# Kernel tuning notes

Measured on AMD Instinct MI355X. Metric: run time of the kernel, lower is better.

## Reference

```python
import jax, jax.numpy as jnp
import numpy as np
from jax import lax

BN_EPS = 1e-5


def _conv_bn_relu(x, W, b, gamma, beta):
    # x: [B, Cin, N]; W: [Cout, Cin]; 1x1 conv == channel GEMM
    y = jnp.einsum('oc,bcn->bon', W, x) + b[None, :, None]
    mean = jnp.mean(y, axis=(0, 2), keepdims=True)
    var = jnp.mean((y - mean) ** 2, axis=(0, 2), keepdims=True)  # biased, torch BN train mode
    y = gamma[None, :, None] * (y - mean) / jnp.sqrt(var + BN_EPS) + beta[None, :, None]
    return jax.nn.relu(y)


def setup_inputs() -> dict:
    key = jax.random.key(0)
    ks = jax.random.split(key, 8)
    B, N1, N2, C1, C2 = 16, 4096, 1024, 128, 256
    Cin, H = C1 + C2, 256  # MLP dims [384, 256, 256]
    inp = {
        'centroids1': jax.random.normal(ks[0], (B, 3, N1), jnp.float32),
        'centroids2': jax.random.normal(ks[1], (B, 3, N2), jnp.float32),
        'features1': jax.random.normal(ks[2], (B, C1, N1), jnp.float32),
        'features2': jax.random.normal(ks[3], (B, C2, N2), jnp.float32),
        'W1': jax.random.normal(ks[4], (H, Cin), jnp.float32) / np.sqrt(Cin),
        'b1': jnp.zeros((H,), jnp.float32),
        'g1': jnp.ones((H,), jnp.float32),
        'be1': jnp.zeros((H,), jnp.float32),
        'W2': jax.random.normal(ks[5], (H, H), jnp.float32) / np.sqrt(H),
        'b2': jnp.zeros((H,), jnp.float32),
        'g2': jnp.ones((H,), jnp.float32),
        'be2': jnp.zeros((H,), jnp.float32),
    }
    return inp


def reference(centroids1, centroids2, features1, features2,
              W1, b1, g1, be1, W2, b2, g2, be2):
    c1 = centroids1.transpose(0, 2, 1)  # [B, N1, 3]
    c2 = centroids2.transpose(0, 2, 1)  # [B, N2, 3]
    f2 = features2.transpose(0, 2, 1)   # [B, N2, C2]

    # pairwise squared distances [B, N1, N2]
    d = (jnp.sum(c1 ** 2, -1)[:, :, None] + jnp.sum(c2 ** 2, -1)[:, None, :]
         - 2.0 * jnp.einsum('bnd,bmd->bnm', c1, c2))

    # 3 nearest neighbors (smallest distances)
    neg_top, idx = lax.top_k(-d, 3)            # idx: [B, N1, 3]
    dist3 = -neg_top
    recip = 1.0 / (dist3 + 1e-8)
    weight = recip / jnp.sum(recip, axis=2, keepdims=True)  # [B, N1, 3]

    gathered = jax.vmap(lambda f, i: f[i])(f2, idx)         # [B, N1, 3, C2]
    interp = jnp.sum(gathered * weight[..., None], axis=2)  # [B, N1, C2]

    feats = jnp.concatenate((features1.transpose(0, 2, 1), interp), axis=-1)  # [B, N1, C1+C2]
    x = feats.transpose(0, 2, 1)  # [B, C1+C2, N1]
    x = _conv_bn_relu(x, W1, b1, g1, be1)
    x = _conv_bn_relu(x, W2, b2, g2, be2)
    return x  # [B, 256, N1]
```

## Files before the change

kernel.cpp:

```cpp
#include <hip/hip_runtime.h>
#include <math.h>

#define N1 4096
#define N2 1024
#define C1 128
#define C2 256
#define CIN 384
#define H 256
#define BATCH 16
#define BN_EPS 1e-5f

typedef __attribute__((ext_vector_type(8))) short bf16x8;
typedef __attribute__((ext_vector_type(4))) float f32x4;

__device__ inline float bf2f(short s) {
    union { unsigned u; float f; } x;
    x.u = ((unsigned)(unsigned short)s) << 16;
    return x.f;
}
__device__ inline short f2bf(float f) {
    union { float f; unsigned u; } x; x.f = f;
    unsigned r = x.u + 0x7fffu + ((x.u >> 16) & 1u);
    return (short)(r >> 16);
}

typedef const __attribute__((address_space(1))) unsigned int guint;
typedef __attribute__((address_space(3))) unsigned int luint;
__device__ inline void gll16(const void* g, void* l) {
    __builtin_amdgcn_global_load_lds((guint*)g, (luint*)l, 16, 0, 0);
}

__global__ __launch_bounds__(256)
void knn_kernel(const float* __restrict__ c1, const float* __restrict__ c2,
                float4* __restrict__ pk) {
    __shared__ __align__(16) float4 sc[N2];
    __shared__ float md[64 * 13];
    __shared__ int   mi[64 * 13];
    const int b = blockIdx.y;
    const float* c2b = c2 + (size_t)b * 3 * N2;
    for (int j = threadIdx.x; j < N2; j += 256) {
        float xx = c2b[j], yy = c2b[N2 + j], zz = c2b[2 * N2 + j];
        sc[j] = make_float4(xx, yy, zz, xx * xx + yy * yy + zz * zz);
    }
    __syncthreads();

    const int t = threadIdx.x;
    const int q = t & 63;
    const int quarter = t >> 6;
    const int n = blockIdx.x * 64 + q;
    const float* c1b = c1 + (size_t)b * 3 * N1;
    const float x = c1b[n], y = c1b[N1 + n], z = c1b[2 * N1 + n];
    const float s1 = x * x + y * y + z * z;

    float d0 = 3.4e38f, d1 = 3.4e38f, d2 = 3.4e38f;
    int i0 = 0, i1 = 0, i2 = 0;
    const int j0 = quarter * 256;
    #pragma unroll 4
    for (int jj = 0; jj < 256; ++jj) {
        const int j = j0 + jj;
        float4 cc = sc[j];
        float dot = x * cc.x + y * cc.y + z * cc.z;
        float d = s1 + cc.w - 2.0f * dot;
        bool c0 = d < d0, c1v = d < d1, c2v = d < d2;
        d2 = c1v ? d1 : (c2v ? d : d2);  i2 = c1v ? i1 : (c2v ? j : i2);
        d1 = c0 ? d0 : (c1v ? d : d1);   i1 = c0 ? i0 : (c1v ? j : i1);
        d0 = c0 ? d  : d0;               i0 = c0 ? j  : i0;
    }
    const int mb = q * 13 + quarter * 3;
    md[mb + 0] = d0; md[mb + 1] = d1; md[mb + 2] = d2;
    mi[mb + 0] = i0; mi[mb + 1] = i1; mi[mb + 2] = i2;
    __syncthreads();

    if (t < 64) {
        float e0 = 3.4e38f, e1 = 3.4e38f, e2 = 3.4e38f;
        int a0 = 0, a1 = 0, a2 = 0;
        #pragma unroll
        for (int r = 0; r < 12; ++r) {
            const int rr = t * 13 + (r / 3) * 3 + (r % 3);
            float d = md[rr]; int j = mi[rr];
            bool c0 = d < e0, c1v = d < e1, c2v = d < e2;
            e2 = c1v ? e1 : (c2v ? d : e2);  a2 = c1v ? a1 : (c2v ? j : a2);
            e1 = c0 ? e0 : (c1v ? d : e1);   a1 = c0 ? a0 : (c1v ? j : a1);
            e0 = c0 ? d  : e0;               a0 = c0 ? j  : a0;
        }
        float r0 = 1.0f / (e0 + 1e-8f);
        float r1 = 1.0f / (e1 + 1e-8f);
        float r2 = 1.0f / (e2 + 1e-8f);
        float rs = r0 + r1 + r2;
        unsigned pack = (unsigned)a0 | ((unsigned)a1 << 10) | ((unsigned)a2 << 20);
        pk[(size_t)b * N1 + n] = make_float4(__uint_as_float(pack), r0 / rs, r1 / rs, r2 / rs);
    }
}

__global__ __launch_bounds__(256)
void prep_w(const float* __restrict__ W, short* __restrict__ Wsw, int K) {
    const int nkb = K >> 3;
    const int id = blockIdx.x * 256 + threadIdx.x;
    if (id >= 256 * nkb) return;
    const int m = id / nkb, kb = id % nkb;
    const float* src = W + (size_t)m * K + kb * 8;
    bf16x8 v;
    #pragma unroll
    for (int j = 0; j < 8; ++j) v[j] = f2bf(src[j]);
    *(bf16x8*)(Wsw + ((size_t)kb * 256 + m) * 8) = v;
}

__global__ __launch_bounds__(256)
void transpose_f2(const float* __restrict__ f2, short* __restrict__ f2t) {
    __shared__ float st[32][33];
    const int j0 = blockIdx.x * 32, c0 = blockIdx.y * 32, b = blockIdx.z;
    const int t = threadIdx.x;
    {
        const int cc = t >> 3, jj = (t & 7) * 4;
        const float* src = f2 + ((size_t)b * C2 + c0 + cc) * N2 + j0 + jj;
        float4 v = *(const float4*)src;
        st[cc][jj + 0] = v.x; st[cc][jj + 1] = v.y;
        st[cc][jj + 2] = v.z; st[cc][jj + 3] = v.w;
    }
    __syncthreads();
    {
        const int j = t >> 3, cb = (t & 7) * 4;
        short4 v = { f2bf(st[cb + 0][j]), f2bf(st[cb + 1][j]),
                     f2bf(st[cb + 2][j]), f2bf(st[cb + 3][j]) };
        *(short4*)(f2t + ((size_t)b * N2 + j0 + j) * C2 + c0 + cb) = v;
    }
}

template<int MODE>
__global__ __launch_bounds__(512)
void gemm_kernel(const short* __restrict__ Wsw,
                 const float* __restrict__ X0, const short* __restrict__ X1,
                 const float4* __restrict__ pk,
                 const float* __restrict__ scale, const float* __restrict__ shift,
                 short* __restrict__ Ykc, float2* __restrict__ P) {
    constexpr int K = (MODE == 0) ? CIN : H;
    constexpr int NT = K / 32;

    __shared__ __align__(16) short A_lds[2][4][256][8];
    __shared__ __align__(16) short B_lds[2][4][128][8];
    __shared__ float sc_s[256], sh_s[256];
    __shared__ float2 pb[256][2];

    const int t = threadIdx.x;
    const int n0 = blockIdx.x * 128;
    const int b  = blockIdx.y;
    const int blkid = b * 32 + blockIdx.x;

    if (MODE == 1 && t < 256) { sc_s[t] = scale[t]; sh_s[t] = shift[t]; }

    const int sn  = t & 127;
    const int skb = t >> 7;
    const int lane = t & 63, wv = t >> 6;
    const int wm = wv >> 1, wn = wv & 1;
    const int l16 = lane & 15, lq = lane >> 4;
    const int am_base = wm * 64 + l16;
    const int bn_base = wn * 64 + l16;

    const float* X0b = (MODE == 0) ? X0 + (size_t)b * C1 * N1 : (const float*)nullptr;
    const short* f2tb = (MODE == 0) ? X1 + (size_t)b * N2 * C2 : (const short*)nullptr;
    const short* y1b  = (MODE == 1) ? X1 + (size_t)b * 32 * N1 * 8 : (const short*)nullptr;

    int gi0 = 0, gi1 = 0, gi2 = 0;
    float gw0 = 0.f, gw1 = 0.f, gw2 = 0.f;
    if (MODE == 0) {
        float4 v = pk[(size_t)b * N1 + n0 + sn];
        unsigned u = __float_as_uint(v.x);
        gi0 = u & 1023; gi1 = (u >> 10) & 1023; gi2 = (u >> 20) & 1023;
        gw0 = v.y; gw1 = v.z; gw2 = v.w;
    }

    f32x4 acc[4][4];
    #pragma unroll
    for (int i = 0; i < 4; ++i)
        #pragma unroll
        for (int j = 0; j < 4; ++j)
            acc[i][j] = (f32x4){0.f, 0.f, 0.f, 0.f};

    auto stageA = [&](int step, int bufi) {
        const short* g = Wsw + (size_t)step * 8192 + wv * 512 + lane * 8;
        short* l = &A_lds[bufi][0][0][0] + wv * 512;
        gll16(g, l);
        gll16(g + 4096, l + 4096);
    };

    auto compute = [&](int bufi) {
        bf16x8 a[4], bb[4];
        #pragma unroll
        for (int f = 0; f < 4; ++f) {
            a[f]  = *(const bf16x8*)&A_lds[bufi][lq][am_base + f * 16][0];
            bb[f] = *(const bf16x8*)&B_lds[bufi][lq][bn_base + f * 16][0];
        }
        #pragma unroll
        for (int i = 0; i < 4; ++i)
            #pragma unroll
            for (int j = 0; j < 4; ++j)
                acc[i][j] = __builtin_amdgcn_mfma_f32_16x16x32_bf16(a[i], bb[j], acc[i][j], 0, 0, 0);
    };

    __syncthreads();

    {
        float pf[8]; bf16x8 pg0, pg1, pg2, py;
        if (MODE == 0) {
            const float* src = X0b + (size_t)(skb * 8) * N1 + n0 + sn;
            #pragma unroll
            for (int j = 0; j < 8; ++j) pf[j] = src[(size_t)j * N1];
        } else {
            py = *(const bf16x8*)(y1b + ((size_t)skb * N1 + n0 + sn) * 8);
        }
        stageA(0, 0);
        bf16x8 pv;
        if (MODE == 0) {
            #pragma unroll
            for (int j = 0; j < 8; ++j) pv[j] = f2bf(pf[j]);
        } else {
            const int gk = skb * 8;
            #pragma unroll
            for (int e = 0; e < 8; ++e)
                pv[e] = f2bf(fmaxf(fmaf(bf2f(py[e]), sc_s[gk + e], sh_s[gk + e]), 0.f));
        }
        *(bf16x8*)&B_lds[0][skb][sn][0] = pv;
        (void)pg0; (void)pg1; (void)pg2;
    }
    __syncthreads();

    int buf = 0;
    for (int s = 0; s < NT; ++s) {
        const bool has_next = (s + 1 < NT);
        const bool nearly = (MODE == 0) && (s + 1 < 4);
        float pf[8]; bf16x8 pg0, pg1, pg2, py;
        if (has_next) {
            if (MODE == 0) {
                if (nearly) {
                    const float* src = X0b + (size_t)((s + 1) * 32 + skb * 8) * N1 + n0 + sn;
                    #pragma unroll
                    for (int j = 0; j < 8; ++j) pf[j] = src[(size_t)j * N1];
                } else {
                    const int c0 = (s + 1) * 32 + skb * 8 - C1;
                    pg0 = *(const bf16x8*)(f2tb + (size_t)gi0 * C2 + c0);
                    pg1 = *(const bf16x8*)(f2tb + (size_t)gi1 * C2 + c0);
                    pg2 = *(const bf16x8*)(f2tb + (size_t)gi2 * C2 + c0);
                }
            } else {
                py = *(const bf16x8*)(y1b + ((size_t)((s + 1) * 4 + skb) * N1 + n0 + sn) * 8);
            }
            stageA(s + 1, buf ^ 1);
        }

        compute(buf);

        if (has_next) {
            bf16x8 pv;
            if (MODE == 0) {
                if (nearly) {
                    #pragma unroll
                    for (int j = 0; j < 8; ++j) pv[j] = f2bf(pf[j]);
                } else {
                    #pragma unroll
                    for (int e = 0; e < 8; ++e)
                        pv[e] = f2bf(fmaf(gw2, bf2f(pg2[e]),
                                     fmaf(gw1, bf2f(pg1[e]), gw0 * bf2f(pg0[e]))));
                }
            } else {
                const int gk = (s + 1) * 32 + skb * 8;
                #pragma unroll
                for (int e = 0; e < 8; ++e)
                    pv[e] = f2bf(fmaxf(fmaf(bf2f(py[e]), sc_s[gk + e], sh_s[gk + e]), 0.f));
            }
            *(bf16x8*)&B_lds[buf ^ 1][skb][sn][0] = pv;
        }
        __syncthreads();
        buf ^= 1;
    }

    short* Yb = Ykc + (size_t)b * 32 * N1 * 8;
    #pragma unroll
    for (int i = 0; i < 4; ++i) {
        const int kb = wm * 8 + i * 2 + (lq >> 1);
        const int kr0 = (lq & 1) * 4;
        #pragma unroll
        for (int j = 0; j < 4; ++j) {
            const int n = n0 + wn * 64 + j * 16 + l16;
            short4 v = { f2bf(acc[i][j][0]), f2bf(acc[i][j][1]),
                         f2bf(acc[i][j][2]), f2bf(acc[i][j][3]) };
            *(short4*)(Yb + ((size_t)kb * N1 + n) * 8 + kr0) = v;
        }
    }

    #pragma unroll
    for (int i = 0; i < 4; ++i) {
        #pragma unroll
        for (int r = 0; r < 4; ++r) {
            float s = 0.f, qq = 0.f;
            #pragma unroll
            for (int j = 0; j < 4; ++j) {
                float xv = acc[i][j][r];
                s += xv; qq += xv * xv;
            }
            #pragma unroll
            for (int msk = 1; msk < 16; msk <<= 1) {
                s  += __shfl_xor(s, msk);
                qq += __shfl_xor(qq, msk);
            }
            if (l16 == 0)
                pb[wm * 64 + i * 16 + lq * 4 + r][wn] = make_float2(s, qq);
        }
    }
    __syncthreads();
    if (t < 256) {
        float2 a = pb[t][0], c = pb[t][1];
        P[(size_t)t * 512 + blkid] = make_float2(a.x + c.x, a.y + c.y);
    }
}

__global__ __launch_bounds__(256)
void bn_reduce(const float2* __restrict__ P, const float* __restrict__ g,
               const float* __restrict__ be, float* __restrict__ scale,
               float* __restrict__ shift) {
    const int c = blockIdx.x, t = threadIdx.x;
    float2 v0 = P[(size_t)c * 512 + t];
    float2 v1 = P[(size_t)c * 512 + 256 + t];
    float s = v0.x + v1.x, q = v0.y + v1.y;
    __shared__ float ss[256], sq[256];
    ss[t] = s; sq[t] = q;
    __syncthreads();
    for (int o = 128; o > 0; o >>= 1) {
        if (t < o) { ss[t] += ss[t + o]; sq[t] += sq[t + o]; }
        __syncthreads();
    }
    if (t == 0) {
        const float inv = 1.0f / (float)(BATCH * N1);
        float mean = ss[0] * inv;
        float var  = sq[0] * inv - mean * mean;
        float sc = g[c] / sqrtf(var + BN_EPS);
        scale[c] = sc;
        shift[c] = be[c] - mean * sc;
    }
}

__global__ __launch_bounds__(256)
void final_bn_relu(const short* __restrict__ y2kc, const float* __restrict__ scale,
                   const float* __restrict__ shift, float* __restrict__ out) {
    const int t = threadIdx.x;
    const int n0 = blockIdx.x * 1024 + t * 4;
    const int kb = blockIdx.y, b = blockIdx.z;
    const short* src = y2kc + ((size_t)(b * 32 + kb) * N1 + n0) * 8;
    bf16x8 v0 = *(const bf16x8*)(src);
    bf16x8 v1 = *(const bf16x8*)(src + 8);
    bf16x8 v2 = *(const bf16x8*)(src + 16);
    bf16x8 v3 = *(const bf16x8*)(src + 24);
    #pragma unroll
    for (int e = 0; e < 8; ++e) {
        const float sc = scale[kb * 8 + e], sh = shift[kb * 8 + e];
        float4 o;
        o.x = fmaxf(fmaf(bf2f(v0[e]), sc, sh), 0.f);
        o.y = fmaxf(fmaf(bf2f(v1[e]), sc, sh), 0.f);
        o.z = fmaxf(fmaf(bf2f(v2[e]), sc, sh), 0.f);
        o.w = fmaxf(fmaf(bf2f(v3[e]), sc, sh), 0.f);
        *(float4*)(out + ((size_t)(b * 256 + kb * 8 + e) * N1) + n0) = o;
    }
}

extern "C" void kernel_launch(void* const* d_in, const int* in_sizes, int n_in,
                              void* d_out, int out_size, void* d_ws, size_t ws_size,
                              hipStream_t stream) {
    const float* c1  = (const float*)d_in[0];
    const float* c2  = (const float*)d_in[1];
    const float* f1  = (const float*)d_in[2];
    const float* f2  = (const float*)d_in[3];
    const float* W1  = (const float*)d_in[4];
    const float* g1  = (const float*)d_in[6];
    const float* be1 = (const float*)d_in[7];
    const float* W2  = (const float*)d_in[8];
    const float* g2  = (const float*)d_in[10];
    const float* be2 = (const float*)d_in[11];
    float* out = (float*)d_out;

    char* ws = (char*)d_ws;
    short*  y2kc = (short*)ws;
    short*  f2t  = (short*)ws;
    short*  W1s  = (short*)(ws + (8u << 20));
    float4* pk   = (float4*)(ws + (9u << 20));
    short*  y1kc = (short*)(ws + (32u << 20));
    short*  W2s  = (short*)(ws + (64u << 20));
    float2* P    = (float2*)(ws + (64u << 20) + (256u << 10));
    float* scale1 = (float*)(ws + (64u << 20) + (256u << 10) + (1u << 20));
    float* shift1 = scale1 + 256;
    float* scale2 = shift1 + 256;
    float* shift2 = scale2 + 256;

    prep_w<<<48, 256, 0, stream>>>(W1, W1s, CIN);
    prep_w<<<32, 256, 0, stream>>>(W2, W2s, H);
    transpose_f2<<<dim3(N2 / 32, C2 / 32, BATCH), 256, 0, stream>>>(f2, f2t);
    knn_kernel<<<dim3(N1 / 64, BATCH), 256, 0, stream>>>(c1, c2, pk);

    gemm_kernel<0><<<dim3(N1 / 128, BATCH), 512, 0, stream>>>(
        W1s, f1, f2t, pk, nullptr, nullptr, y1kc, P);
    bn_reduce<<<256, 256, 0, stream>>>(P, g1, be1, scale1, shift1);

    gemm_kernel<1><<<dim3(N1 / 128, BATCH), 512, 0, stream>>>(
        W2s, nullptr, y1kc, nullptr, scale1, shift1, y2kc, P);
    bn_reduce<<<256, 256, 0, stream>>>(P, g2, be2, scale2, shift2);

    final_bn_relu<<<dim3(N1 / 1024, 32, BATCH), 256, 0, stream>>>(y2kc, scale2, shift2, out);
}
```

Baseline: 148.8 us.

## Split GEMM output channels across two 256-thread blocks with grouped block ordering

Each GEMM block now computes 128 of the 256 output channels with 4 waves instead of all 256 with 8 waves. This doubles the grid to 1024 blocks and uses a grouped ordering so the two channel halves of the same tile run near each other and share the B operand in cache. Each thread now stages two B sub-chunks, and the MFMA fragment indexing was remapped. The aim is more blocks per CU and better occupancy, at the cost of gathering and converting the B tile (including the KNN interpolation) twice per spatial tile.

```diff
diff --git a/kernel.cpp b/kernel.cpp
--- a/kernel.cpp
+++ b/kernel.cpp
@@ -127,7 +127,7 @@
 }
 
 template<int MODE>
-__global__ __launch_bounds__(512)
+__global__ __launch_bounds__(256, 4)
 void gemm_kernel(const short* __restrict__ Wsw,
                  const float* __restrict__ X0, const short* __restrict__ X1,
                  const float4* __restrict__ pk,
@@ -136,27 +136,30 @@
     constexpr int K = (MODE == 0) ? CIN : H;
     constexpr int NT = K / 32;
 
-    __shared__ __align__(16) short A_lds[2][4][256][8];
+    __shared__ __align__(16) short A_lds[2][4][128][8];
     __shared__ __align__(16) short B_lds[2][4][128][8];
     __shared__ float sc_s[256], sh_s[256];
-    __shared__ float2 pb[256][2];
+    __shared__ float2 pb[128][2];
 
     const int t = threadIdx.x;
-    const int n0 = blockIdx.x * 128;
-    const int b  = blockIdx.y;
-    const int blkid = b * 32 + blockIdx.x;
+    const int d = blockIdx.x;
+    const int grp = d >> 4, rem = d & 15;
+    const int mh = rem >> 3;
+    const int pair = grp * 8 + (rem & 7);
+    const int nt = pair & 31, b = pair >> 5;
+    const int n0 = nt * 128;
 
     if (MODE == 1 && t < 256) { sc_s[t] = scale[t]; sh_s[t] = shift[t]; }
 
-    const int sn  = t & 127;
-    const int skb = t >> 7;
+    const int sn = t & 127;
+    const int kh = t >> 7;
     const int lane = t & 63, wv = t >> 6;
     const int wm = wv >> 1, wn = wv & 1;
     const int l16 = lane & 15, lq = lane >> 4;
     const int am_base = wm * 64 + l16;
     const int bn_base = wn * 64 + l16;
 
-    const float* X0b = (MODE == 0) ? X0 + (size_t)b * C1 * N1 : (const float*)nullptr;
+    const float* X0b  = (MODE == 0) ? X0 + (size_t)b * C1 * N1 : (const float*)nullptr;
     const short* f2tb = (MODE == 0) ? X1 + (size_t)b * N2 * C2 : (const short*)nullptr;
     const short* y1b  = (MODE == 1) ? X1 + (size_t)b * 32 * N1 * 8 : (const short*)nullptr;
 
@@ -177,18 +180,22 @@
             acc[i][j] = (f32x4){0.f, 0.f, 0.f, 0.f};
 
     auto stageA = [&](int step, int bufi) {
-        const short* g = Wsw + (size_t)step * 8192 + wv * 512 + lane * 8;
-        short* l = &A_lds[bufi][0][0][0] + wv * 512;
-        gll16(g, l);
-        gll16(g + 4096, l + 4096);
+        #pragma unroll
+        for (int i = 0; i < 2; ++i) {
+            const int c = i * 256 + t;
+            const int kb = c >> 7, mm = c & 127;
+            const short* g = Wsw + (((size_t)step * 4 + kb) * 256 + mh * 128 + mm) * 8;
+            short* l = &A_lds[bufi][0][0][0] + (size_t)c * 8;
+            gll16(g, l);
+        }
     };
 
     auto compute = [&](int bufi) {
         bf16x8 a[4], bb[4];
         #pragma unroll
         for (int f = 0; f < 4; ++f) {
-            a[f]  = *(const bf16x8*)&A_lds[bufi][lq][am_base + f * 16][0];
-            bb[f] = *(const bf16x8*)&B_lds[bufi][lq][bn_base + f * 16][0];
+            a[f]  = *(const bf16x8*)&A_lds[bufi][lq][am_base + ((f & 1) << 4) + ((f >> 1) << 5)][0];
+            bb[f] = *(const bf16x8*)&B_lds[bufi][lq][bn_base + ((f & 1) << 4) + ((f >> 1) << 5)][0];
         }
         #pragma unroll
         for (int i = 0; i < 4; ++i)
@@ -200,83 +207,101 @@
     __syncthreads();
 
     {
-        float pf[8]; bf16x8 pg0, pg1, pg2, py;
-        if (MODE == 0) {
-            const float* src = X0b + (size_t)(skb * 8) * N1 + n0 + sn;
-            #pragma unroll
-            for (int j = 0; j < 8; ++j) pf[j] = src[(size_t)j * N1];
-        } else {
-            py = *(const bf16x8*)(y1b + ((size_t)skb * N1 + n0 + sn) * 8);
+        float pf[2][8]; bf16x8 pg[2][3]; bf16x8 py[2];
+        #pragma unroll
+        for (int ci = 0; ci < 2; ++ci) {
+            const int skb = kh + ci * 2;
+            if (MODE == 0) {
+                const float* src = X0b + (size_t)(skb * 8) * N1 + n0 + sn;
+                #pragma unroll
+                for (int j = 0; j < 8; ++j) pf[ci][j] = src[(size_t)j * N1];
+            } else {
+                py[ci] = *(const bf16x8*)(y1b + ((size_t)skb * N1 + n0 + sn) * 8);
+            }
         }
         stageA(0, 0);
-        bf16x8 pv;
-        if (MODE == 0) {
-            #pragma unroll
-            for (int j = 0; j < 8; ++j) pv[j] = f2bf(pf[j]);
-        } else {
-            const int gk = skb * 8;
-            #pragma unroll
-            for (int e = 0; e < 8; ++e)
-                pv[e] = f2bf(fmaxf(fmaf(bf2f(py[e]), sc_s[gk + e], sh_s[gk + e]), 0.f));
-        }
-        *(bf16x8*)&B_lds[0][skb][sn][0] = pv;
-        (void)pg0; (void)pg1; (void)pg2;
+        #pragma unroll
+        for (int ci = 0; ci < 2; ++ci) {
+            const int skb = kh + ci * 2;
+            bf16x8 pv;
+            if (MODE == 0) {
+                #pragma unroll
+                for (int j = 0; j < 8; ++j) pv[j] = f2bf(pf[ci][j]);
+            } else {
+                const int gk = skb * 8;
+                #pragma unroll
+                for (int e = 0; e < 8; ++e)
+                    pv[e] = f2bf(fmaxf(fmaf(bf2f(py[ci][e]), sc_s[gk + e], sh_s[gk + e]), 0.f));
+            }
+            *(bf16x8*)&B_lds[0][skb][sn][0] = pv;
+        }
+        (void)pg;
     }
     __syncthreads();
 
     int buf = 0;
     for (int s = 0; s < NT; ++s) {
         const bool has_next = (s + 1 < NT);
-        const bool nearly = (MODE == 0) && (s + 1 < 4);
-        float pf[8]; bf16x8 pg0, pg1, pg2, py;
+        float pf[2][8]; bf16x8 pg[2][3]; bf16x8 py[2];
         if (has_next) {
-            if (MODE == 0) {
-                if (nearly) {
-                    const float* src = X0b + (size_t)((s + 1) * 32 + skb * 8) * N1 + n0 + sn;
-                    #pragma unroll
-                    for (int j = 0; j < 8; ++j) pf[j] = src[(size_t)j * N1];
+            const int sx = s + 1;
+            #pragma unroll
+            for (int ci = 0; ci < 2; ++ci) {
+                const int skb = kh + ci * 2;
+                const int gk = sx * 32 + skb * 8;
+                if (MODE == 0) {
+                    if (gk < C1) {
+                        const float* src = X0b + (size_t)gk * N1 + n0 + sn;
+                        #pragma unroll
+                        for (int j = 0; j < 8; ++j) pf[ci][j] = src[(size_t)j * N1];
+                    } else {
+                        const int c0 = gk - C1;
+                        pg[ci][0] = *(const bf16x8*)(f2tb + (size_t)gi0 * C2 + c0);
+                        pg[ci][1] = *(const bf16x8*)(f2tb + (size_t)gi1 * C2 + c0);
+                        pg[ci][2] = *(const bf16x8*)(f2tb + (size_t)gi2 * C2 + c0);
+                    }
                 } else {
-                    const int c0 = (s + 1) * 32 + skb * 8 - C1;
-                    pg0 = *(const bf16x8*)(f2tb + (size_t)gi0 * C2 + c0);
-                    pg1 = *(const bf16x8*)(f2tb + (size_t)gi1 * C2 + c0);
-                    pg2 = *(const bf16x8*)(f2tb + (size_t)gi2 * C2 + c0);
+                    py[ci] = *(const bf16x8*)(y1b + ((size_t)(sx * 4 + skb) * N1 + n0 + sn) * 8);
                 }
-            } else {
-                py = *(const bf16x8*)(y1b + ((size_t)((s + 1) * 4 + skb) * N1 + n0 + sn) * 8);
-            }
-            stageA(s + 1, buf ^ 1);
+            }
+            stageA(sx, buf ^ 1);
         }
 
         compute(buf);
 
         if (has_next) {
-            bf16x8 pv;
-            if (MODE == 0) {
-                if (nearly) {
-                    #pragma unroll
-                    for (int j = 0; j < 8; ++j) pv[j] = f2bf(pf[j]);
+            const int sx = s + 1;
+            #pragma unroll
+            for (int ci = 0; ci < 2; ++ci) {
+                const int skb = kh + ci * 2;
+                const int gk = sx * 32 + skb * 8;
+                bf16x8 pv;
+                if (MODE == 0) {
+                    if (gk < C1) {
+                        #pragma unroll
+                        for (int j = 0; j < 8; ++j) pv[j] = f2bf(pf[ci][j]);
+                    } else {
+                        #pragma unroll
+                        for (int e = 0; e < 8; ++e)
+                            pv[e] = f2bf(fmaf(gw2, bf2f(pg[ci][2][e]),
+                                         fmaf(gw1, bf2f(pg[ci][1][e]), gw0 * bf2f(pg[ci][0][e]))));
+                    }
                 } else {
                     #pragma unroll
                     for (int e = 0; e < 8; ++e)
-                        pv[e] = f2bf(fmaf(gw2, bf2f(pg2[e]),
-                                     fmaf(gw1, bf2f(pg1[e]), gw0 * bf2f(pg0[e]))));
+                        pv[e] = f2bf(fmaxf(fmaf(bf2f(py[ci][e]), sc_s[gk + e], sh_s[gk + e]), 0.f));
                 }
-            } else {
-                const int gk = (s + 1) * 32 + skb * 8;
-                #pragma unroll
-                for (int e = 0; e < 8; ++e)
-                    pv[e] = f2bf(fmaxf(fmaf(bf2f(py[e]), sc_s[gk + e], sh_s[gk + e]), 0.f));
-            }
-            *(bf16x8*)&B_lds[buf ^ 1][skb][sn][0] = pv;
+                *(bf16x8*)&B_lds[buf ^ 1][skb][sn][0] = pv;
+            }
         }
         __syncthreads();
         buf ^= 1;
     }
 
-    short* Yb = Ykc + (size_t)b * 32 * N1 * 8;
+    short* Yb = Ykc + (size_t)b * (K == CIN ? 32 : 32) * 0 + (size_t)b * 32 * N1 * 8;
     #pragma unroll
     for (int i = 0; i < 4; ++i) {
-        const int kb = wm * 8 + i * 2 + (lq >> 1);
+        const int kb = mh * 16 + wm * 8 + i * 2 + (lq >> 1);
         const int kr0 = (lq & 1) * 4;
         #pragma unroll
         for (int j = 0; j < 4; ++j) {
@@ -307,9 +332,9 @@
         }
     }
     __syncthreads();
-    if (t < 256) {
+    if (t < 128) {
         float2 a = pb[t][0], c = pb[t][1];
-        P[(size_t)t * 512 + blkid] = make_float2(a.x + c.x, a.y + c.y);
+        P[(size_t)(mh * 128 + t) * 512 + b * 32 + nt] = make_float2(a.x + c.x, a.y + c.y);
     }
 }
 
@@ -394,11 +419,11 @@
     transpose_f2<<<dim3(N2 / 32, C2 / 32, BATCH), 256, 0, stream>>>(f2, f2t);
     knn_kernel<<<dim3(N1 / 64, BATCH), 256, 0, stream>>>(c1, c2, pk);
 
-    gemm_kernel<0><<<dim3(N1 / 128, BATCH), 512, 0, stream>>>(
+    gemm_kernel<0><<<1024, 256, 0, stream>>>(
         W1s, f1, f2t, pk, nullptr, nullptr, y1kc, P);
     bn_reduce<<<256, 256, 0, stream>>>(P, g1, be1, scale1, shift1);
 
-    gemm_kernel<1><<<dim3(N1 / 128, BATCH), 512, 0, stream>>>(
+    gemm_kernel<1><<<1024, 256, 0, stream>>>(
         W2s, nullptr, y1kc, nullptr, scale1, shift1, y2kc, P);
     bn_reduce<<<256, 256, 0, stream>>>(P, g2, be2, scale2, shift2);
 
```

New measurement: 303.0 us. 2.04x slower.
